# Kernel optimization log

Hardware: AMD Instinct MI355X
Metric: run time of the kernel (lower is better)

## Reference

```python
import jax, jax.numpy as jnp
from jax import lax
import numpy as np


def _tv1d_row(y, lam):
    """Condat's direct O(n) 1D TV-L1 prox (TV1D_denoise) on one row.
    Solves min_x 0.5*||x-y||^2 + lam * sum|x_{i+1}-x_i|.
    State machine translation of Condat (2013) Algorithm 1.
    """
    W = y.shape[0]
    idx = jnp.arange(W)
    dt = y.dtype

    def write(out, lo, hi, v):
        # out[lo:hi+1] = v  (masked, jit-friendly)
        return jnp.where((idx >= lo) & (idx <= hi), v, out)

    def cond_fn(s):
        return ~s[9]

    def body_fn(s):
        out, k, k0, km, kp, umin, umax, vmin, vmax, done = s
        T = jnp.array(True)
        F = jnp.array(False)

        def branchA(_):  # k == W-1
            def a1(_):  # umin < 0: flush negative segment at vmin
                o = write(out, k0, km, vmin)
                k0n = km + 1
                vminn = y[jnp.minimum(k0n, W - 1)]
                return (o, k0n, k0n, k0n, kp, lam, vminn + lam - vmax, vminn, vmax, F)

            def a2(_):  # umax > 0: flush positive segment at vmax
                o = write(out, k0, kp, vmax)
                k0n = kp + 1
                vmaxn = y[jnp.minimum(k0n, W - 1)]
                return (o, k0n, k0n, km, k0n, vmaxn - lam - vmin, -lam, vmin, vmaxn, F)

            def a3(_):  # terminate
                v = vmin + umin / (k - k0 + 1).astype(dt)
                o = write(out, k0, k, v)
                return (o, k, k0, km, kp, umin, umax, v, vmax, T)

            return lax.cond(umin < 0, a1,
                            lambda _: lax.cond(umax > 0, a2, a3, None), None)

        def branchB(_):  # k < W-1
            yn = y[jnp.minimum(k + 1, W - 1)]
            umin_t = umin + yn - vmin
            umax_t = umax + yn - vmax

            def b1(_):  # negative jump: flush at vmin, restart
                o = write(out, k0, km, vmin)
                k0n = km + 1
                vminn = y[jnp.minimum(k0n, W - 1)]
                return (o, k0n, k0n, k0n, k0n, lam, -lam, vminn, vminn + 2 * lam, F)

            def b2(_):  # positive jump: flush at vmax, restart
                o = write(out, k0, kp, vmax)
                k0n = kp + 1
                vmaxn = y[jnp.minimum(k0n, W - 1)]
                return (o, k0n, k0n, k0n, k0n, lam, -lam, vmaxn - 2 * lam, vmaxn, F)

            def b3(_):  # extend current segment
                kn = k + 1
                denom = (kn - k0 + 1).astype(dt)
                hit_min = umin_t >= lam
                hit_max = umax_t <= -lam
                vminn = jnp.where(hit_min, vmin + (umin_t - lam) / denom, vmin)
                uminn = jnp.where(hit_min, lam, umin_t)
                kmn = jnp.where(hit_min, kn, km)
                vmaxn = jnp.where(hit_max, vmax + (umax_t + lam) / denom, vmax)
                umaxn = jnp.where(hit_max, -lam, umax_t)
                kpn = jnp.where(hit_max, kn, kp)
                return (out, kn, k0, kmn, kpn, uminn, umaxn, vminn, vmaxn, F)

            return lax.cond(umin_t < -lam, b1,
                            lambda _: lax.cond(umax_t > lam, b2, b3, None), None)

        return lax.cond(k == W - 1, branchA, branchB, None)

    z = jnp.int32(0)
    init = (jnp.zeros_like(y), z, z, z, z, lam, -lam, y[0] - lam, y[0] + lam, jnp.array(False))
    return lax.while_loop(cond_fn, body_fn, init)[0]


def tv1d_batch(y_flat, lam_rows):
    return jax.vmap(_tv1d_row)(y_flat, lam_rows)


def setup_inputs() -> dict:
    key = jax.random.key(0)
    N, C, H, W = 8, 3, 256, 512
    y = jax.random.normal(key, (N, C, H, W), dtype=jnp.float32)
    # learned lmbd parameter initialized so that softplus(lmbd) = 0.5 (lmbd_init=0.5, lmbd_zero<0 -> offset 0)
    lmbd = jnp.full((1, C), float(np.log(np.expm1(0.5))), dtype=jnp.float32)
    return {"y": y, "lmbd": lmbd}


def reference(y, lmbd):
    N, C, H, W = y.shape
    lam = jax.nn.softplus(lmbd)  # get_lmbd_val with lmbd_offset = 0
    lam_rows = jnp.broadcast_to(lam.reshape(1, C, 1), (N, C, H)).reshape(-1)  # (N*C*H,)
    x = tv1d_batch(y.reshape(-1, W), lam_rows)
    return x.reshape(N, C, H, W)
```

## Files before the change

kernel.cpp:

```cpp
#include <hip/hip_runtime.h>
#include <math.h>

#define TVW 512
#define TVH 256
#define TVC 3
#define WPB 2
#define BLOCK (WPB * 64)

__global__ __launch_bounds__(BLOCK)
void tv1d_condat_wave_kernel(const float* __restrict__ y,
                             const float* __restrict__ lmbd,
                             float* __restrict__ out,
                             int total_rows) {
    __shared__ __align__(16) float buf[WPB * TVW + 4];
    __shared__ float rtab[520];
    const int tid  = threadIdx.x;
    const int wave = tid >> 6;
    const int lane = tid & 63;
    const int base_row = blockIdx.x * WPB;
    const int row = base_row + wave;

    {
        float4* b4 = (float4*)buf;
        const float4* s4 = (const float4*)(y + (size_t)base_row * TVW);
        #pragma unroll
        for (int i = 0; i < (WPB * TVW / 4); i += BLOCK)
            b4[i + tid] = s4[i + tid];
    }
    for (int i = tid; i < 520; i += BLOCK)
        rtab[i] = 1.0f / (float)(i == 0 ? 1 : i);
    __syncthreads();

    if (row < total_rows) {
        const int c = (row / TVH) % TVC;
        float lam = log1pf(expf(lmbd[c]));
        lam = __uint_as_float(__builtin_amdgcn_readfirstlane(__float_as_uint(lam)));
        const float nlam   = -lam;
        const float twolam = 2.0f * lam;
        float* x = buf + wave * TVW;

        int k0 = 0, km = 0, kp = 0;
        float vmin = x[0] - lam, vmax = x[0] + lam;
        float umin = lam, umax = nlam;

        for (int guard = 0; guard < 4096; ++guard) {
            int trips = (TVW - 1) - k0;
            if (trips < 0) trips = 0;

            float yn = x[k0 + 1];
            float rn = 0.5f;
            const float* xpp = x + (k0 + 2);
            const float* rpp = rtab + 3;
            const int kb = k0 + 1;

            float umin_t = 0.0f, umax_t = 0.0f;
            int t = 0;
            for (; t < trips; ++t) {
                const float yn2 = xpp[t];
                const float rn2 = rpp[t];
                umin_t = umin + yn - vmin;
                umax_t = umax + yn - vmax;
                if (__ballot(fmaxf(-umin_t, umax_t) > lam)) break;
                const int kc = kb + t;
                km = __ballot(umin_t >= lam)  ? kc : km;
                kp = __ballot(umax_t <= nlam) ? kc : kp;
                const float umin_n = fminf(umin_t, lam);
                const float umax_n = fmaxf(umax_t, nlam);
                vmin = fmaf(umin_t - umin_n, rn, vmin);
                vmax = fmaf(umax_t - umax_n, rn, vmax);
                umin = umin_n;
                umax = umax_n;
                yn = yn2; rn = rn2;
            }

            if (t < trips) {
                if (__ballot(umin_t < nlam)) {
                    for (int p = k0 + lane; p <= km; p += 64) x[p] = vmin;
                    k0 = km + 1;
                    km = kp = k0;
                    vmin = x[k0];
                    vmax = vmin + twolam;
                } else {
                    for (int p = k0 + lane; p <= kp; p += 64) x[p] = vmax;
                    k0 = kp + 1;
                    km = kp = k0;
                    vmax = x[k0];
                    vmin = vmax - twolam;
                }
                umin = lam; umax = nlam;
            } else {
                if (__ballot(umin < 0.0f)) {
                    const int pe = km < TVW - 1 ? km : TVW - 1;
                    for (int p = k0 + lane; p <= pe; p += 64) x[p] = vmin;
                    k0 = km + 1;
                    km = k0;
                    vmin = x[k0 < TVW ? k0 : TVW - 1];
                    umax = vmin + lam - vmax;
                    umin = lam;
                } else if (__ballot(umax > 0.0f)) {
                    const int pe = kp < TVW - 1 ? kp : TVW - 1;
                    for (int p = k0 + lane; p <= pe; p += 64) x[p] = vmax;
                    k0 = kp + 1;
                    kp = k0;
                    vmax = x[k0 < TVW ? k0 : TVW - 1];
                    umin = vmax + nlam - vmin;
                    umax = nlam;
                } else {
                    const float v = vmin + umin * rtab[trips + 1];
                    for (int p = k0 + lane; p < TVW; p += 64) x[p] = v;
                    break;
                }
            }
        }
    }
    __syncthreads();

    {
        float4* b4 = (float4*)buf;
        float4* d4 = (float4*)(out + (size_t)base_row * TVW);
        #pragma unroll
        for (int i = 0; i < (WPB * TVW / 4); i += BLOCK)
            d4[i + tid] = b4[i + tid];
    }
}

extern "C" void kernel_launch(void* const* d_in, const int* in_sizes, int n_in,
                              void* d_out, int out_size, void* d_ws, size_t ws_size,
                              hipStream_t stream) {
    const float* y    = (const float*)d_in[0];
    const float* lmbd = (const float*)d_in[1];
    float* out = (float*)d_out;

    const int total_rows = in_sizes[0] / TVW;
    const int grid = (total_rows + WPB - 1) / WPB;
    tv1d_condat_wave_kernel<<<grid, BLOCK, 0, stream>>>(y, lmbd, out, total_rows);
}
```

Before: 276.2 us.

## Split Condat min/max tracks across half-waves using negated row copy

```diff
diff --git a/kernel.cpp b/kernel.cpp
--- a/kernel.cpp
+++ b/kernel.cpp
@@ -12,23 +12,33 @@
                              const float* __restrict__ lmbd,
                              float* __restrict__ out,
                              int total_rows) {
-    __shared__ __align__(16) float buf[WPB * TVW + 4];
+    __shared__ __align__(16) float buf [WPB * TVW + 4];
+    __shared__ __align__(16) float bneg[WPB * TVW + 4];
     __shared__ float rtab[520];
     const int tid  = threadIdx.x;
     const int wave = tid >> 6;
     const int lane = tid & 63;
+    const bool hi  = lane >= 32;
     const int base_row = blockIdx.x * WPB;
     const int row = base_row + wave;
 
     {
         float4* b4 = (float4*)buf;
+        float4* n4 = (float4*)bneg;
         const float4* s4 = (const float4*)(y + (size_t)base_row * TVW);
         #pragma unroll
-        for (int i = 0; i < (WPB * TVW / 4); i += BLOCK)
-            b4[i + tid] = s4[i + tid];
+        for (int i = 0; i < (WPB * TVW / 4); i += BLOCK) {
+            const float4 v = s4[i + tid];
+            b4[i + tid] = v;
+            n4[i + tid] = make_float4(-v.x, -v.y, -v.z, -v.w);
+        }
     }
     for (int i = tid; i < 520; i += BLOCK)
         rtab[i] = 1.0f / (float)(i == 0 ? 1 : i);
+    if (tid < 4) {
+        buf [WPB * TVW + tid] = 0.0f;
+        bneg[WPB * TVW + tid] = 0.0f;
+    }
     __syncthreads();
 
     if (row < total_rows) {
@@ -38,76 +48,93 @@
         const float nlam   = -lam;
         const float twolam = 2.0f * lam;
         float* x = buf + wave * TVW;
+        const float* xs = hi ? (bneg + wave * TVW) : (buf + wave * TVW);
+        const float cneg = hi ? twolam : 0.0f;
+        const float cpos = hi ? 0.0f : twolam;
 
         int k0 = 0, km = 0, kp = 0;
-        float vmin = x[0] - lam, vmax = x[0] + lam;
-        float umin = lam, umax = nlam;
+        float v = xs[0] - lam;
+        float u = lam;
+        float yn = xs[1];
 
         for (int guard = 0; guard < 4096; ++guard) {
-            int trips = (TVW - 1) - k0;
-            if (trips < 0) trips = 0;
-
-            float yn = x[k0 + 1];
+            const int trips = (TVW - 1) - k0;
             float rn = 0.5f;
-            const float* xpp = x + (k0 + 2);
+            const float* xpp = xs + (k0 + 2);
             const float* rpp = rtab + 3;
             const int kb = k0 + 1;
 
-            float umin_t = 0.0f, umax_t = 0.0f;
+            unsigned long long jb = 0;
             int t = 0;
             for (; t < trips; ++t) {
                 const float yn2 = xpp[t];
                 const float rn2 = rpp[t];
-                umin_t = umin + yn - vmin;
-                umax_t = umax + yn - vmax;
-                if (__ballot(fmaxf(-umin_t, umax_t) > lam)) break;
+                const float u_t = u + yn - v;
+                jb = __ballot(u_t < nlam);
+                if (jb) break;
+                const unsigned long long cb = __ballot(u_t >= lam);
                 const int kc = kb + t;
-                km = __ballot(umin_t >= lam)  ? kc : km;
-                kp = __ballot(umax_t <= nlam) ? kc : kp;
-                const float umin_n = fminf(umin_t, lam);
-                const float umax_n = fmaxf(umax_t, nlam);
-                vmin = fmaf(umin_t - umin_n, rn, vmin);
-                vmax = fmaf(umax_t - umax_n, rn, vmax);
-                umin = umin_n;
-                umax = umax_n;
+                km = (unsigned)(cb)       ? kc : km;
+                kp = (unsigned)(cb >> 32) ? kc : kp;
+                const float u_n = fminf(u_t, lam);
+                v = fmaf(u_t - u_n, rn, v);
+                u = u_n;
                 yn = yn2; rn = rn2;
             }
 
             if (t < trips) {
-                if (__ballot(umin_t < nlam)) {
-                    for (int p = k0 + lane; p <= km; p += 64) x[p] = vmin;
-                    k0 = km + 1;
-                    km = kp = k0;
-                    vmin = x[k0];
-                    vmax = vmin + twolam;
+                if ((unsigned)jb) {
+                    const int k0n = km + 1;
+                    const float fv  = __shfl(v, 0);
+                    const float nvl = xs[k0n];
+                    const float ynn = xs[k0n + 1];
+                    for (int p = k0 + lane; p <= km; p += 64) x[p] = fv;
+                    k0 = k0n; km = kp = k0n;
+                    v = nvl - cneg;
+                    yn = ynn;
                 } else {
-                    for (int p = k0 + lane; p <= kp; p += 64) x[p] = vmax;
-                    k0 = kp + 1;
-                    km = kp = k0;
-                    vmax = x[k0];
-                    vmin = vmax - twolam;
+                    const int k0n = kp + 1;
+                    const float fv  = -__shfl(v, 32);
+                    const float nvl = xs[k0n];
+                    const float ynn = xs[k0n + 1];
+                    for (int p = k0 + lane; p <= kp; p += 64) x[p] = fv;
+                    k0 = k0n; km = kp = k0n;
+                    v = nvl - cpos;
+                    yn = ynn;
                 }
-                umin = lam; umax = nlam;
+                u = lam;
             } else {
-                if (__ballot(umin < 0.0f)) {
+                const unsigned long long bb = __ballot(u < 0.0f);
+                if ((unsigned)bb) {
+                    const int k0n = km + 1;
+                    const float fv = __shfl(v, 0);
+                    float nvl = 0.0f, ynn = 0.0f;
+                    if (k0n < TVW) { nvl = xs[k0n]; ynn = xs[k0n + 1]; }
                     const int pe = km < TVW - 1 ? km : TVW - 1;
-                    for (int p = k0 + lane; p <= pe; p += 64) x[p] = vmin;
-                    k0 = km + 1;
-                    km = k0;
-                    vmin = x[k0 < TVW ? k0 : TVW - 1];
-                    umax = vmin + lam - vmax;
-                    umin = lam;
-                } else if (__ballot(umax > 0.0f)) {
+                    for (int p = k0 + lane; p <= pe; p += 64) x[p] = fv;
+                    if (k0n >= TVW) break;
+                    const float tt = nvl - lam;
+                    u = hi ? (tt - v) : lam;
+                    v = hi ? v : nvl;
+                    yn = ynn;
+                    k0 = k0n; km = k0n;
+                } else if ((unsigned)(bb >> 32)) {
+                    const int k0n = kp + 1;
+                    const float fv = -__shfl(v, 32);
+                    float nvl = 0.0f, ynn = 0.0f;
+                    if (k0n < TVW) { nvl = xs[k0n]; ynn = xs[k0n + 1]; }
                     const int pe = kp < TVW - 1 ? kp : TVW - 1;
-                    for (int p = k0 + lane; p <= pe; p += 64) x[p] = vmax;
-                    k0 = kp + 1;
-                    kp = k0;
-                    vmax = x[k0 < TVW ? k0 : TVW - 1];
-                    umin = vmax + nlam - vmin;
-                    umax = nlam;
+                    for (int p = k0 + lane; p <= pe; p += 64) x[p] = fv;
+                    if (k0n >= TVW) break;
+                    const float tt = nvl - lam;
+                    u = hi ? lam : (tt - v);
+                    v = hi ? nvl : v;
+                    yn = ynn;
+                    k0 = k0n; kp = k0n;
                 } else {
-                    const float v = vmin + umin * rtab[trips + 1];
-                    for (int p = k0 + lane; p < TVW; p += 64) x[p] = v;
+                    const float vt = fmaf(u, rtab[trips + 1], v);
+                    const float fv = __shfl(vt, 0);
+                    for (int p = k0 + lane; p < TVW; p += 64) x[p] = fv;
                     break;
                 }
             }
```

Result: no change. 276.0 us (-0.1%).
